# Kernel tuning notes

Measured on AMD Instinct MI355X. Metric: run time of the kernel, lower is better.

The kernel has to match this reference:

```python
import jax, jax.numpy as jnp
import numpy as np

N_HEADS = 8
OUT_F = 64  # per-head output features (concat=True)
LEAKY_SLOPE = 0.2
MASK_FILL = -1000000000.0
L2_EPS = 1e-12  # tf.nn.l2_normalize epsilon


def setup_inputs() -> dict:
    key = jax.random.key(0)
    k1, k2, k3 = jax.random.split(key, 3)
    B, N, F_IN = 8, 1024, 256
    h = jax.random.normal(k1, (B, N, F_IN), dtype=jnp.float32)
    # glorot-uniform-ish scaling for params
    W = jax.random.normal(k2, (F_IN, OUT_F * N_HEADS), dtype=jnp.float32) * 0.05
    a = jax.random.normal(k3, (N_HEADS, 2 * OUT_F, 1), dtype=jnp.float32) * 0.05
    return {"h": h, "W": W, "a": a}


def reference(h, W, a):
    B, N, _ = h.shape
    H, D = N_HEADS, OUT_F

    # dynamic adjacency from cosine similarity threshold (tf.nn.l2_normalize semantics)
    inv_norm = jax.lax.rsqrt(jnp.maximum(jnp.sum(h * h, axis=-1, keepdims=True), L2_EPS))
    h_norm = h * inv_norm
    sim = jnp.einsum('bnd,bmd->bnm', h_norm, h_norm)  # [B,N,N]
    adj = jnp.where(sim > 0.5, 1.0, 0.0)

    # feature projection, split into heads: [B,H,N,D]
    ht = jnp.matmul(h, W).reshape(B, N, H, D).transpose(0, 2, 1, 3)

    # additive dual scores
    src = jnp.einsum('bhnd,hdf->bhnf', ht, a[:, :D, :])   # [B,H,N,1]
    tgt = jnp.einsum('bhnd,hdf->bhnf', ht, a[:, D:, :])   # [B,H,N,1]
    e = src + tgt.transpose(0, 1, 3, 2)                   # [B,H,N,N]
    e = jnp.where(e > 0, e, LEAKY_SLOPE * e)              # leaky relu

    # mask by adjacency, softmax over last axis
    masked = jnp.where(adj[:, None, :, :] > 0, e, MASK_FILL)
    attention = jax.nn.softmax(masked, axis=-1)

    h_prime = jnp.einsum('bhij,bhjd->bhid', attention, ht)  # [B,H,N,D]
    # faithful to original: reshape [B,H,N,D] -> [B,N,H*D] WITHOUT transpose
    return h_prime.reshape(B, N, H * D)
```

## Files before the change

### kernel.cpp

```cpp
#include <hip/hip_runtime.h>
#include <hip/hip_bf16.h>
#include <math.h>

#define B 8
#define N 1024
#define F 256
#define H 8
#define D 64
#define HD 512

typedef __attribute__((ext_vector_type(8))) short bf16x8;
typedef __attribute__((ext_vector_type(16))) float f32x16;

__device__ __forceinline__ ushort f2bf(float x) {
    __hip_bfloat16 b = __float2bfloat16(x);
    return *reinterpret_cast<ushort*>(&b);
}

__device__ __forceinline__ void gl_lds16(const void* g, void* l) {
    __builtin_amdgcn_global_load_lds(
        (__attribute__((address_space(1))) void*)const_cast<void*>(g),
        (__attribute__((address_space(3))) void*)l, 16, 0, 0);
}

#define SWZ(r, byte) ((byte) ^ (((r) & 7) << 4))

__global__ __launch_bounds__(256) void k_prep(const float* __restrict__ h,
                                              const float* __restrict__ W,
                                              ushort* __restrict__ hn,
                                              ushort* __restrict__ Wt,
                                              float* __restrict__ nrm) {
    if (blockIdx.x < 2048) {
        int row = (blockIdx.x * 256 + threadIdx.x) >> 6;
        int lane = threadIdx.x & 63;
        float4 v = *reinterpret_cast<const float4*>(h + (size_t)row * F + lane * 4);
        float s = v.x * v.x + v.y * v.y + v.z * v.z + v.w * v.w;
        #pragma unroll
        for (int off = 32; off; off >>= 1) s += __shfl_xor(s, off, 64);
        float sn = fmaxf(s, 1e-12f);
        float inv = rsqrtf(sn);
        ushort4 on;
        on.x = f2bf(v.x * inv); on.y = f2bf(v.y * inv);
        on.z = f2bf(v.z * inv); on.w = f2bf(v.w * inv);
        *reinterpret_cast<ushort4*>(hn + (size_t)row * F + lane * 4) = on;
        if (lane == 0) nrm[row] = sn * inv;
    } else {
        int idx = (blockIdx.x - 2048) * 256 + threadIdx.x;
        int k = idx >> 9;
        int n = idx & 511;
        Wt[(size_t)n * F + k] = f2bf(W[idx]);
    }
}

__global__ __launch_bounds__(256) void k_gemm(const ushort* __restrict__ hn,
                                              const ushort* __restrict__ Wt,
                                              const float* __restrict__ nrm,
                                              const float* __restrict__ a,
                                              float* __restrict__ ht,
                                              float* __restrict__ out,
                                              float* __restrict__ src,
                                              float* __restrict__ tgt,
                                              unsigned* __restrict__ adj) {
    __shared__ __align__(16) ushort As[128 * 64];
    __shared__ __align__(16) ushort Bs[128 * 64];
    __shared__ float norms[64];
    const int x = blockIdx.x & 7;
    const int q = blockIdx.x >> 3;
    const int t = threadIdx.x;
    const int lane = t & 63;
    const int w = t >> 6;
    const int wr = w >> 1, wc = w & 1;
    const int lr = lane >> 3;
    const int lg = ((lane & 7) ^ lr) << 4;

    if (q < 64) {
        const int sid = x * 64 + q;
        const int m0 = (sid >> 2) * 64;
        const int n0 = (sid & 3) * 128;
        if (t < 64) norms[t] = nrm[m0 + t];
        const char* aB = (const char*)hn + (size_t)(m0 + lr) * 512 + lg;
        const char* bB = (const char*)Wt + (size_t)(n0 + lr) * 512 + lg;
        f32x16 acc[2] = {};

        for (int f2 = 0; f2 < 512; f2 += 128) {
            __syncthreads();
            #pragma unroll
            for (int k = 0; k < 2; ++k) {
                int c = w * 2 + k;
                gl_lds16(aB + (size_t)c * 4096 + f2, (char*)As + c * 1024);
            }
            #pragma unroll
            for (int k = 0; k < 4; ++k) {
                int c = w * 4 + k;
                gl_lds16(bB + (size_t)c * 4096 + f2, (char*)Bs + c * 1024);
            }
            __syncthreads();
            #pragma unroll
            for (int kc = 0; kc < 4; ++kc) {
                int kb = kc * 32 + (lane >> 5) * 16;
                int ra = wr * 32 + (lane & 31);
                bf16x8 af = *reinterpret_cast<const bf16x8*>((char*)As + ra * 128 + SWZ(ra, kb));
                #pragma unroll
                for (int tc = 0; tc < 2; ++tc) {
                    int rb = wc * 64 + tc * 32 + (lane & 31);
                    bf16x8 bf = *reinterpret_cast<const bf16x8*>((char*)Bs + rb * 128 + SWZ(rb, kb));
                    acc[tc] = __builtin_amdgcn_mfma_f32_32x32x16_bf16(af, bf, acc[tc], 0, 0, 0);
                }
            }
        }
        const int head = (n0 >> 6) + wc;
        #pragma unroll
        for (int tc = 0; tc < 2; ++tc) {
            int d = tc * 32 + (lane & 31);
            #pragma unroll
            for (int reg = 0; reg < 16; ++reg) {
                int ml = wr * 32 + (reg & 3) + 8 * (reg >> 2) + 4 * (lane >> 5);
                int m = m0 + ml;
                int b = m >> 10, n = m & 1023;
                float v = acc[tc][reg] * norms[ml];
                size_t idx = ((size_t)((b * H + head) * N + n)) * D + d;
                ht[idx] = v;
                out[idx] = v;
            }
        }
        const int dl = lane & 31;
        float as0 = a[head * 128 + dl];
        float as1 = a[head * 128 + 32 + dl];
        float at0 = a[head * 128 + 64 + dl];
        float at1 = a[head * 128 + 96 + dl];
        #pragma unroll
        for (int reg = 0; reg < 16; ++reg) {
            float s  = acc[0][reg] * as0 + acc[1][reg] * as1;
            float tg = acc[0][reg] * at0 + acc[1][reg] * at1;
            #pragma unroll
            for (int off = 16; off; off >>= 1) {
                s  += __shfl_xor(s, off, 64);
                tg += __shfl_xor(tg, off, 64);
            }
            if (dl == 0) {
                int ml = wr * 32 + (reg & 3) + 8 * (reg >> 2) + 4 * (lane >> 5);
                int m = m0 + ml;
                int b = m >> 10, n = m & 1023;
                float sc = norms[ml];
                size_t idx = (size_t)(b * H + head) * N + n;
                src[idx] = s * sc;
                tgt[idx] = tg * sc;
            }
        }
    } else {
        const int b = x;
        int pp = q - 64;
        int ti = 0;
        while (pp >= 8 - ti) { pp -= 8 - ti; ++ti; }
        const int tj = ti + pp;
        const int i0 = ti * 128, j0 = tj * 128;
        const char* hbB = (const char*)hn + (size_t)b * N * 512;
        const char* aB = hbB + (size_t)(i0 + lr) * 512 + lg;
        const char* bB = hbB + (size_t)(j0 + lr) * 512 + lg;
        f32x16 acc[2][2] = {};

        for (int f2 = 0; f2 < 512; f2 += 128) {
            __syncthreads();
            #pragma unroll
            for (int k = 0; k < 4; ++k) {
                int c = w * 4 + k;
                gl_lds16(aB + (size_t)c * 4096 + f2, (char*)As + c * 1024);
                gl_lds16(bB + (size_t)c * 4096 + f2, (char*)Bs + c * 1024);
            }
            __syncthreads();
            #pragma unroll
            for (int kc = 0; kc < 4; ++kc) {
                int kb = kc * 32 + (lane >> 5) * 16;
                bf16x8 af[2], bfr[2];
                #pragma unroll
                for (int tr = 0; tr < 2; ++tr) {
                    int r = wr * 64 + tr * 32 + (lane & 31);
                    af[tr] = *reinterpret_cast<const bf16x8*>((char*)As + r * 128 + SWZ(r, kb));
                }
                #pragma unroll
                for (int tc = 0; tc < 2; ++tc) {
                    int r = wc * 64 + tc * 32 + (lane & 31);
                    bfr[tc] = *reinterpret_cast<const bf16x8*>((char*)Bs + r * 128 + SWZ(r, kb));
                }
                #pragma unroll
                for (int tr = 0; tr < 2; ++tr)
                    #pragma unroll
                    for (int tc = 0; tc < 2; ++tc)
                        acc[tr][tc] = __builtin_amdgcn_mfma_f32_32x32x16_bf16(af[tr], bfr[tc], acc[tr][tc], 0, 0, 0);
            }
        }
        #pragma unroll
        for (int tr = 0; tr < 2; ++tr) {
            #pragma unroll
            for (int tc = 0; tc < 2; ++tc) {
                int wordcol = (j0 + wc * 64 + tc * 32) >> 5;
                int rb0 = i0 + wr * 64 + tr * 32;
                unsigned tw = 0;
                #pragma unroll
                for (int reg = 0; reg < 16; ++reg) {
                    bool pr = acc[tr][tc][reg] > 0.5f;
                    unsigned long long msk = __ballot(pr);
                    int rbase = rb0 + (reg & 3) + 8 * (reg >> 2);
                    if (lane == 0)
                        adj[(size_t)(b * N + rbase) * 32 + wordcol] = (unsigned)msk;
                    if (lane == 32)
                        adj[(size_t)(b * N + rbase + 4) * 32 + wordcol] = (unsigned)(msk >> 32);
                    tw |= (pr ? 1u : 0u) << ((reg & 3) + 8 * (reg >> 2) + 4 * (lane >> 5));
                }
                if (ti != tj) {
                    tw |= (unsigned)__shfl_xor((int)tw, 32, 64);
                    if (lane < 32) {
                        int cj = j0 + wc * 64 + tc * 32 + lane;
                        adj[(size_t)(b * N + cj) * 32 + (rb0 >> 5)] = tw;
                    }
                }
            }
        }
    }
}

__global__ void k_attn(const float* __restrict__ ht, const float* __restrict__ src,
                       const float* __restrict__ tgt, const unsigned* __restrict__ adj,
                       float* __restrict__ out) {
    int row = (blockIdx.x * 256 + threadIdx.x) >> 6;
    int lane = threadIdx.x & 63;
    if (row >= B * N) return;
    const unsigned* arow = adj + (size_t)row * 32;
    unsigned myword = (lane < 32) ? arow[lane] : 0u;
    int cnt = __popc(myword);
    #pragma unroll
    for (int off = 32; off; off >>= 1) cnt += __shfl_xor(cnt, off, 64);
    if (cnt <= 1) return;

    unsigned long long nz = __ballot(myword != 0u);
    int b = row >> 10, i = row & 1023;
    for (int hh = 0; hh < H; ++hh) {
        int bh = b * H + hh;
        const float* htb = ht + (size_t)bh * N * D;
        const float* tgtb = tgt + (size_t)bh * N;
        float s_i = src[(size_t)bh * N + i];
        float m = -INFINITY, l = 0.f, acc = 0.f;
        unsigned long long qz = nz;
        while (qz) {
            int wt = __builtin_ctzll(qz);
            qz &= qz - 1;
            unsigned word = (unsigned)__shfl((int)myword, wt, 64);
            while (word) {
                int jl = __builtin_ctz(word);
                word &= word - 1;
                int j = wt * 32 + jl;
                float e = s_i + tgtb[j];
                e = e > 0.f ? e : 0.2f * e;
                float mn = fmaxf(m, e);
                float scl = __expf(m - mn);
                float p   = __expf(e - mn);
                l = l * scl + p;
                acc = acc * scl + p * htb[(size_t)j * D + lane];
                m = mn;
            }
        }
        out[((size_t)bh * N + i) * D + lane] = acc / l;
    }
}

extern "C" void kernel_launch(void* const* d_in, const int* in_sizes, int n_in,
                              void* d_out, int out_size, void* d_ws, size_t ws_size,
                              hipStream_t stream) {
    const float* h = (const float*)d_in[0];
    const float* W = (const float*)d_in[1];
    const float* a = (const float*)d_in[2];
    float* out = (float*)d_out;

    char* ws = (char*)d_ws;
    unsigned* adj = (unsigned*)(ws + 0);
    float*    src = (float*)(ws + 1048576);
    float*    tgt = (float*)(ws + 1310720);
    float*    ht  = (float*)(ws + 1572864);
    ushort*   hn  = (ushort*)(ws + 18350080);
    ushort*   Wt  = (ushort*)(ws + 22544384);
    float*    nrm = (float*)(ws + 22806528);

    k_prep<<<dim3(2560), 256, 0, stream>>>(h, W, hn, Wt, nrm);
    k_gemm<<<dim3(800), 256, 0, stream>>>(hn, Wt, nrm, a, ht, out, src, tgt, adj);
    k_attn<<<dim3((B * N) / 4), 256, 0, stream>>>(ht, src, tgt, adj, out);
}
```

Before: 37.86 us.

## Enlarge projection GEMM tiles to 128x128 and store projected features as bf16

Projection blocks now compute 128x128 output tiles with a 2x2 MFMA arrangement per wave, halving their count and reusing each A/B fragment across two MFMAs. Block indexing is remapped so odd q slots go to similarity tiles, cutting the grid from 800 to 544 blocks. The intermediate ht buffer is written as bf16 and converted back in the attention kernel, halving its write and gather traffic. The cost is reduced precision in the aggregated features, plus fewer, heavier projection blocks.

```diff
diff --git a/kernel.cpp b/kernel.cpp
--- a/kernel.cpp
+++ b/kernel.cpp
@@ -15,6 +15,10 @@
 __device__ __forceinline__ ushort f2bf(float x) {
     __hip_bfloat16 b = __float2bfloat16(x);
     return *reinterpret_cast<ushort*>(&b);
+}
+__device__ __forceinline__ float bf2f(ushort u) {
+    __hip_bfloat16 b = *reinterpret_cast<__hip_bfloat16*>(&u);
+    return __bfloat162float(b);
 }
 
 __device__ __forceinline__ void gl_lds16(const void* g, void* l) {
@@ -56,14 +60,14 @@
                                               const ushort* __restrict__ Wt,
                                               const float* __restrict__ nrm,
                                               const float* __restrict__ a,
-                                              float* __restrict__ ht,
+                                              ushort* __restrict__ ht,
                                               float* __restrict__ out,
                                               float* __restrict__ src,
                                               float* __restrict__ tgt,
                                               unsigned* __restrict__ adj) {
     __shared__ __align__(16) ushort As[128 * 64];
     __shared__ __align__(16) ushort Bs[128 * 64];
-    __shared__ float norms[64];
+    __shared__ float norms[128];
     const int x = blockIdx.x & 7;
     const int q = blockIdx.x >> 3;
     const int t = threadIdx.x;
@@ -73,54 +77,63 @@
     const int lr = lane >> 3;
     const int lg = ((lane & 7) ^ lr) << 4;
 
-    if (q < 64) {
-        const int sid = x * 64 + q;
-        const int m0 = (sid >> 2) * 64;
+    const bool is_proj = (q < 64) && ((q & 1) == 0);
+
+    if (is_proj) {
+        const int sid = x * 32 + (q >> 1);
+        const int m0 = (sid >> 2) * 128;
         const int n0 = (sid & 3) * 128;
-        if (t < 64) norms[t] = nrm[m0 + t];
+        if (t < 128) norms[t] = nrm[m0 + t];
         const char* aB = (const char*)hn + (size_t)(m0 + lr) * 512 + lg;
         const char* bB = (const char*)Wt + (size_t)(n0 + lr) * 512 + lg;
-        f32x16 acc[2] = {};
+        f32x16 acc[2][2] = {};
 
         for (int f2 = 0; f2 < 512; f2 += 128) {
             __syncthreads();
             #pragma unroll
-            for (int k = 0; k < 2; ++k) {
-                int c = w * 2 + k;
-                gl_lds16(aB + (size_t)c * 4096 + f2, (char*)As + c * 1024);
-            }
-            #pragma unroll
             for (int k = 0; k < 4; ++k) {
                 int c = w * 4 + k;
+                gl_lds16(aB + (size_t)c * 4096 + f2, (char*)As + c * 1024);
                 gl_lds16(bB + (size_t)c * 4096 + f2, (char*)Bs + c * 1024);
             }
             __syncthreads();
             #pragma unroll
             for (int kc = 0; kc < 4; ++kc) {
                 int kb = kc * 32 + (lane >> 5) * 16;
-                int ra = wr * 32 + (lane & 31);
-                bf16x8 af = *reinterpret_cast<const bf16x8*>((char*)As + ra * 128 + SWZ(ra, kb));
+                bf16x8 af[2], bfr[2];
+                #pragma unroll
+                for (int tr = 0; tr < 2; ++tr) {
+                    int r = wr * 64 + tr * 32 + (lane & 31);
+                    af[tr] = *reinterpret_cast<const bf16x8*>((char*)As + r * 128 + SWZ(r, kb));
+                }
                 #pragma unroll
                 for (int tc = 0; tc < 2; ++tc) {
-                    int rb = wc * 64 + tc * 32 + (lane & 31);
-                    bf16x8 bf = *reinterpret_cast<const bf16x8*>((char*)Bs + rb * 128 + SWZ(rb, kb));
-                    acc[tc] = __builtin_amdgcn_mfma_f32_32x32x16_bf16(af, bf, acc[tc], 0, 0, 0);
-                }
+                    int r = wc * 64 + tc * 32 + (lane & 31);
+                    bfr[tc] = *reinterpret_cast<const bf16x8*>((char*)Bs + r * 128 + SWZ(r, kb));
+                }
+                #pragma unroll
+                for (int tr = 0; tr < 2; ++tr)
+                    #pragma unroll
+                    for (int tc = 0; tc < 2; ++tc)
+                        acc[tr][tc] = __builtin_amdgcn_mfma_f32_32x32x16_bf16(af[tr], bfr[tc], acc[tr][tc], 0, 0, 0);
             }
         }
         const int head = (n0 >> 6) + wc;
         #pragma unroll
-        for (int tc = 0; tc < 2; ++tc) {
-            int d = tc * 32 + (lane & 31);
-            #pragma unroll
-            for (int reg = 0; reg < 16; ++reg) {
-                int ml = wr * 32 + (reg & 3) + 8 * (reg >> 2) + 4 * (lane >> 5);
-                int m = m0 + ml;
-                int b = m >> 10, n = m & 1023;
-                float v = acc[tc][reg] * norms[ml];
-                size_t idx = ((size_t)((b * H + head) * N + n)) * D + d;
-                ht[idx] = v;
-                out[idx] = v;
+        for (int tr = 0; tr < 2; ++tr) {
+            #pragma unroll
+            for (int tc = 0; tc < 2; ++tc) {
+                int d = tc * 32 + (lane & 31);
+                #pragma unroll
+                for (int reg = 0; reg < 16; ++reg) {
+                    int ml = wr * 64 + tr * 32 + (reg & 3) + 8 * (reg >> 2) + 4 * (lane >> 5);
+                    int m = m0 + ml;
+                    int b = m >> 10, n = m & 1023;
+                    float v = acc[tr][tc][reg] * norms[ml];
+                    size_t idx = ((size_t)((b * H + head) * N + n)) * D + d;
+                    ht[idx] = f2bf(v);
+                    out[idx] = v;
+                }
             }
         }
         const int dl = lane & 31;
@@ -129,27 +142,30 @@
         float at0 = a[head * 128 + 64 + dl];
         float at1 = a[head * 128 + 96 + dl];
         #pragma unroll
-        for (int reg = 0; reg < 16; ++reg) {
-            float s  = acc[0][reg] * as0 + acc[1][reg] * as1;
-            float tg = acc[0][reg] * at0 + acc[1][reg] * at1;
-            #pragma unroll
-            for (int off = 16; off; off >>= 1) {
-                s  += __shfl_xor(s, off, 64);
-                tg += __shfl_xor(tg, off, 64);
-            }
-            if (dl == 0) {
-                int ml = wr * 32 + (reg & 3) + 8 * (reg >> 2) + 4 * (lane >> 5);
-                int m = m0 + ml;
-                int b = m >> 10, n = m & 1023;
-                float sc = norms[ml];
-                size_t idx = (size_t)(b * H + head) * N + n;
-                src[idx] = s * sc;
-                tgt[idx] = tg * sc;
+        for (int tr = 0; tr < 2; ++tr) {
+            #pragma unroll
+            for (int reg = 0; reg < 16; ++reg) {
+                float s  = acc[tr][0][reg] * as0 + acc[tr][1][reg] * as1;
+                float tg = acc[tr][0][reg] * at0 + acc[tr][1][reg] * at1;
+                #pragma unroll
+                for (int off = 16; off; off >>= 1) {
+                    s  += __shfl_xor(s, off, 64);
+                    tg += __shfl_xor(tg, off, 64);
+                }
+                if (dl == 0) {
+                    int ml = wr * 64 + tr * 32 + (reg & 3) + 8 * (reg >> 2) + 4 * (lane >> 5);
+                    int m = m0 + ml;
+                    int b = m >> 10, n = m & 1023;
+                    float sc = norms[ml];
+                    size_t idx = (size_t)(b * H + head) * N + n;
+                    src[idx] = s * sc;
+                    tgt[idx] = tg * sc;
+                }
             }
         }
     } else {
         const int b = x;
-        int pp = q - 64;
+        int pp = (q < 64) ? (q >> 1) : (32 + (q - 64));
         int ti = 0;
         while (pp >= 8 - ti) { pp -= 8 - ti; ++ti; }
         const int tj = ti + pp;
@@ -219,7 +235,7 @@
     }
 }
 
-__global__ void k_attn(const float* __restrict__ ht, const float* __restrict__ src,
+__global__ void k_attn(const ushort* __restrict__ ht, const float* __restrict__ src,
                        const float* __restrict__ tgt, const unsigned* __restrict__ adj,
                        float* __restrict__ out) {
     int row = (blockIdx.x * 256 + threadIdx.x) >> 6;
@@ -236,7 +252,7 @@
     int b = row >> 10, i = row & 1023;
     for (int hh = 0; hh < H; ++hh) {
         int bh = b * H + hh;
-        const float* htb = ht + (size_t)bh * N * D;
+        const ushort* htb = ht + (size_t)bh * N * D;
         const float* tgtb = tgt + (size_t)bh * N;
         float s_i = src[(size_t)bh * N + i];
         float m = -INFINITY, l = 0.f, acc = 0.f;
@@ -255,7 +271,7 @@
                 float scl = __expf(m - mn);
                 float p   = __expf(e - mn);
                 l = l * scl + p;
-                acc = acc * scl + p * htb[(size_t)j * D + lane];
+                acc = acc * scl + p * bf2f(htb[(size_t)j * D + lane]);
                 m = mn;
             }
         }
@@ -275,12 +291,12 @@
     unsigned* adj = (unsigned*)(ws + 0);
     float*    src = (float*)(ws + 1048576);
     float*    tgt = (float*)(ws + 1310720);
-    float*    ht  = (float*)(ws + 1572864);
-    ushort*   hn  = (ushort*)(ws + 18350080);
-    ushort*   Wt  = (ushort*)(ws + 22544384);
-    float*    nrm = (float*)(ws + 22806528);
+    ushort*   ht  = (ushort*)(ws + 1572864);
+    ushort*   hn  = (ushort*)(ws + 9961472);
+    ushort*   Wt  = (ushort*)(ws + 14155776);
+    float*    nrm = (float*)(ws + 14417920);
 
     k_prep<<<dim3(2560), 256, 0, stream>>>(h, W, hn, Wt, nrm);
-    k_gemm<<<dim3(800), 256, 0, stream>>>(hn, Wt, nrm, a, ht, out, src, tgt, adj);
+    k_gemm<<<dim3(544), 256, 0, stream>>>(hn, Wt, nrm, a, ht, out, src, tgt, adj);
     k_attn<<<dim3((B * N) / 4), 256, 0, stream>>>(ht, src, tgt, adj, out);
 }
```

Measured after the change: 39.42 us. 1.04x slower.
